# Kernel optimization log

Measured on AMD Instinct MI355X. Metric: run time of the kernel, lower is better.

The kernel has to match this reference:

```python
import jax, jax.numpy as jnp
import numpy as np


def _layernorm(x, g, b, eps=1e-5):
    mu = jnp.mean(x, axis=-1, keepdims=True)
    var = jnp.mean(jnp.square(x - mu), axis=-1, keepdims=True)
    return (x - mu) * jax.lax.rsqrt(var + eps) * g + b


def setup_inputs() -> dict:
    key = jax.random.key(0)
    ks = jax.random.split(key, 8)
    B, S, E, K, H = 32, 64, 768, 36, 4
    w = 0.02
    return {
        "x": jax.random.normal(ks[0], (B, S, E), dtype=jnp.float32),
        "y": jax.random.normal(ks[1], (B * S, K, E), dtype=jnp.float32),
        "ln_gamma": jnp.ones((H, E), jnp.float32),
        "ln_beta": jnp.zeros((H, E), jnp.float32),
        "W1": jax.random.normal(ks[2], (H, E, E), dtype=jnp.float32) * w,
        "b1": jnp.zeros((H, E), jnp.float32),
        "W2x": jax.random.normal(ks[3], (H, E), dtype=jnp.float32) * w,  # first half of Linear(2E,1)
        "W2y": jax.random.normal(ks[4], (H, E), dtype=jnp.float32) * w,  # second half of Linear(2E,1)
        "b2": jnp.zeros((H,), jnp.float32),
        "Wm": jax.random.normal(ks[5], (H * E, E), dtype=jnp.float32) * w,
        "bm": jnp.zeros((E,), jnp.float32),
        "select_indegree_num": 36,
    }


def reference(x, y, ln_gamma, ln_beta, W1, b1, W2x, W2y, b2, Wm, bm, select_indegree_num):
    # x: [B,S,E], y: [B*S,K,E]; dropout layers are identity in eval mode.
    B, S, E = x.shape
    H = ln_gamma.shape[0]
    xf = x.reshape(B * S, E)
    outs = []
    for h in range(H):
        # shared linear1 (LayerNorm + Linear) applied to both x and y
        x_ = _layernorm(xf, ln_gamma[h], ln_beta[h]) @ W1[h] + b1[h]          # [BS,E]
        y_ = _layernorm(y, ln_gamma[h], ln_beta[h]) @ W1[h] + b1[h]           # [BS,K,E]
        logit = (x_ @ W2x[h])[:, None] + y_ @ W2y[h] + b2[h]                  # [BS,K]
        prob = jax.nn.softmax(logit, axis=1)                                   # softmax over neighbors
        a = jnp.einsum('nk,nke->ne', prob, y_)                                 # weighted sum, [BS,E]
        outs.append(jax.nn.gelu(xf + a))                                       # GELU(x + a)
    cat = jnp.concatenate(outs, axis=-1)                                       # [BS,H*E]
    res = jax.nn.gelu(cat @ Wm + bm).reshape(B, S, E)
    return x + res  # has_residual=True
```

## Files before the change

kernel.cpp:

```cpp
#include <hip/hip_runtime.h>
#include <hip/hip_bf16.h>
#include <math.h>

#define EE 768
#define HH 4
#define KK 36
#define BSN 2048

typedef __attribute__((ext_vector_type(8))) short short8;
typedef __attribute__((ext_vector_type(4))) short short4v;
typedef __attribute__((ext_vector_type(4))) float float4v;

__device__ inline short f2bf(float x){
  return __builtin_bit_cast(short, __float2bfloat16(x));
}
__device__ inline float bf2f(short s){
  return __bfloat162float(__builtin_bit_cast(__hip_bfloat16, s));
}
__device__ inline float gelu_tanh(float x){
  float t = tanhf(0.79788456080286536f * (x + 0.044715f * x * x * x));
  return 0.5f * x * (1.0f + t);
}

__global__ __launch_bounds__(256) void k_prep(const float* __restrict__ W1,
                                              const float* __restrict__ W2y,
                                              const float* __restrict__ g,
                                              const float* __restrict__ b1,
                                              const float* __restrict__ Wm,
                                              float* __restrict__ v,
                                              float* __restrict__ b1p,
                                              short* __restrict__ W1t,
                                              short* __restrict__ Wmt){
  __shared__ float tile[32][33];
  const int b = blockIdx.x;

  if (b < 768){
    const int wid  = b * 4 + (threadIdx.x >> 6);
    const int lane = threadIdx.x & 63;
    const int h = wid / EE, e = wid % EE;
    const float* W  = W1 + ((size_t)h * EE + e) * EE;
    const float* wy = W2y + h * EE;
    float acc = 0.f;
    #pragma unroll
    for (int j = 0; j < 12; ++j){
      int f = lane + 64 * j;
      acc += W[f] * wy[f];
    }
    #pragma unroll
    for (int off = 32; off; off >>= 1) acc += __shfl_xor(acc, off);
    if (lane == 0) v[h * EE + e] = g[h * EE + e] * acc;

    int idx = b * 256 + threadIdx.x;
    if (idx < HH * EE) b1p[idx] = b1[idx];
  } else if (b < 3072){
    const int bb = b - 768;
    const int et = bb % 24, ft = (bb / 24) % 24, h = bb / 576;
    const int e0 = et * 32, f0 = ft * 32;
    const int tx = threadIdx.x & 31, ty = threadIdx.x >> 5;
    const float* W = W1 + (size_t)h * EE * EE;
    #pragma unroll
    for (int i = 0; i < 4; ++i){
      int e = e0 + ty + 8 * i;
      tile[ty + 8 * i][tx] = W[(size_t)e * EE + f0 + tx] * g[h * EE + e];
    }
    __syncthreads();
    #pragma unroll
    for (int i = 0; i < 4; ++i){
      int f = f0 + ty + 8 * i;
      W1t[((size_t)h * EE + f) * EE + e0 + tx] = f2bf(tile[tx][ty + 8 * i]);
    }
  } else {
    const int bb = b - 3072;
    const int ct = bb % 96, ft = bb / 96;
    const int c0 = ct * 32, f0 = ft * 32;
    const int tx = threadIdx.x & 31, ty = threadIdx.x >> 5;
    #pragma unroll
    for (int i = 0; i < 4; ++i){
      tile[ty + 8 * i][tx] = Wm[(size_t)(c0 + ty + 8 * i) * EE + f0 + tx];
    }
    __syncthreads();
    #pragma unroll
    for (int i = 0; i < 4; ++i){
      Wmt[(size_t)(f0 + ty + 8 * i) * (HH * EE) + c0 + tx] = f2bf(tile[tx][ty + 8 * i]);
    }
  }
}

__global__ __launch_bounds__(256) void k_b1p_acc(const float* __restrict__ W1,
                                                 const float* __restrict__ beta,
                                                 float* __restrict__ b1p){
  const int h   = blockIdx.x >> 6;
  const int ec0 = (blockIdx.x & 63) * 12;
  const float* W  = W1 + (size_t)h * EE * EE;
  const float* bt = beta + h * EE;
  const int f = threadIdx.x;
  float a0 = 0.f, a1 = 0.f, a2 = 0.f;
  #pragma unroll
  for (int e = ec0; e < ec0 + 12; ++e){
    float be = bt[e];
    const float* row = W + (size_t)e * EE;
    a0 += be * row[f];
    a1 += be * row[f + 256];
    a2 += be * row[f + 512];
  }
  atomicAdd(&b1p[h * EE + f],       a0);
  atomicAdd(&b1p[h * EE + f + 256], a1);
  atomicAdd(&b1p[h * EE + f + 512], a2);
}

__global__ __launch_bounds__(256) void k_pass_y(const float* __restrict__ y,
                                                const float* __restrict__ v,
                                                short* __restrict__ p_y){
  const int wave = threadIdx.x >> 6, lane = threadIdx.x & 63;
  const int n = blockIdx.x * 4 + wave;
  const float* base = y + (size_t)n * KK * EE + 4 * lane;

  float4v vreg[HH][3];
  #pragma unroll
  for (int h = 0; h < HH; ++h)
    #pragma unroll
    for (int j = 0; j < 3; ++j)
      vreg[h][j] = *(const float4v*)(v + h * EE + 4 * lane + 256 * j);

  float4v acc[HH][3];
  #pragma unroll
  for (int h = 0; h < HH; ++h)
    #pragma unroll
    for (int j = 0; j < 3; ++j)
      acc[h][j] = (float4v){0.f, 0.f, 0.f, 0.f};
  float m[HH], l[HH];
  #pragma unroll
  for (int h = 0; h < HH; ++h){ m[h] = -INFINITY; l[h] = 0.f; }

  float4v bufA[3], bufB[3];
  #pragma unroll
  for (int j = 0; j < 3; ++j) bufA[j] = *(const float4v*)(base + 256 * j);
  #pragma unroll
  for (int j = 0; j < 3; ++j) bufB[j] = *(const float4v*)(base + EE + 256 * j);

  #pragma unroll 2
  for (int k = 0; k < KK; ++k){
    float4v cur[3];
    #pragma unroll
    for (int j = 0; j < 3; ++j) cur[j] = bufA[j];
    #pragma unroll
    for (int j = 0; j < 3; ++j) bufA[j] = bufB[j];
    if (k + 2 < KK){
      const float* rp = base + (size_t)(k + 2) * EE;
      #pragma unroll
      for (int j = 0; j < 3; ++j) bufB[j] = *(const float4v*)(rp + 256 * j);
    }

    float s = 0.f, s2 = 0.f;
    #pragma unroll
    for (int j = 0; j < 3; ++j)
      #pragma unroll
      for (int c = 0; c < 4; ++c){ float t = cur[j][c]; s += t; s2 += t * t; }
    #pragma unroll
    for (int off = 32; off; off >>= 1){
      s  += __shfl_xor(s, off);
      s2 += __shfl_xor(s2, off);
    }
    const float mu = s * (1.f / EE);
    const float rs = rsqrtf(s2 * (1.f / EE) - mu * mu + 1e-5f);

    float d[HH] = {0.f, 0.f, 0.f, 0.f};
    #pragma unroll
    for (int j = 0; j < 3; ++j)
      #pragma unroll
      for (int c = 0; c < 4; ++c){
        float t = (cur[j][c] - mu) * rs;
        cur[j][c] = t;
        d[0] += t * vreg[0][j][c];
        d[1] += t * vreg[1][j][c];
        d[2] += t * vreg[2][j][c];
        d[3] += t * vreg[3][j][c];
      }
    #pragma unroll
    for (int off = 32; off; off >>= 1){
      d[0] += __shfl_xor(d[0], off);
      d[1] += __shfl_xor(d[1], off);
      d[2] += __shfl_xor(d[2], off);
      d[3] += __shfl_xor(d[3], off);
    }

    #pragma unroll
    for (int h = 0; h < HH; ++h){
      if (d[h] > m[h]){
        float sc = __expf(m[h] - d[h]);
        l[h] *= sc;
        #pragma unroll
        for (int j = 0; j < 3; ++j)
          #pragma unroll
          for (int c = 0; c < 4; ++c) acc[h][j][c] *= sc;
        m[h] = d[h];
      }
      float w = __expf(d[h] - m[h]);
      l[h] += w;
      #pragma unroll
      for (int j = 0; j < 3; ++j)
        #pragma unroll
        for (int c = 0; c < 4; ++c) acc[h][j][c] += w * cur[j][c];
    }
  }

  #pragma unroll
  for (int h = 0; h < HH; ++h){
    const float inv = 1.f / l[h];
    #pragma unroll
    for (int j = 0; j < 3; ++j){
      short4v pk;
      #pragma unroll
      for (int c = 0; c < 4; ++c) pk[c] = f2bf(acc[h][j][c] * inv);
      *(short4v*)(p_y + ((size_t)h * BSN + n) * EE + 4 * lane + 256 * j) = pk;
    }
  }
}

template<int MODE>
__global__ __launch_bounds__(256) void k_gemm(const short* __restrict__ A,
                                              const short* __restrict__ Bt,
                                              const float* __restrict__ addv,
                                              const float* __restrict__ x,
                                              void* __restrict__ out,
                                              int Kdim, size_t strideA, size_t strideB){
  __shared__ short As[2][64][72];
  __shared__ short Bs[2][64][72];
  const int z = blockIdx.z;
  const short* Ah = A + strideA * z;
  const short* Bh = Bt + strideB * z;
  const int kbeg = 0, kend = Kdim;

  const int tid = threadIdx.x;
  const int wave = tid >> 6, lane = tid & 63;
  const int quad = lane >> 4, l16 = lane & 15;
  const int m0 = blockIdx.x * 64, n0 = blockIdx.y * 64;
  const int r = tid >> 3, c8 = (tid & 7) * 8;

  float4v acc[4];
  #pragma unroll
  for (int t = 0; t < 4; ++t) acc[t] = (float4v){0.f, 0.f, 0.f, 0.f};

  const short* Ap0 = Ah + (size_t)(m0 + r) * Kdim + c8;
  const short* Ap1 = Ah + (size_t)(m0 + r + 32) * Kdim + c8;
  const short* Bp0 = Bh + (size_t)(n0 + r) * Kdim + c8;
  const short* Bp1 = Bh + (size_t)(n0 + r + 32) * Kdim + c8;

  short8 ra0 = *(const short8*)(Ap0 + kbeg);
  short8 ra1 = *(const short8*)(Ap1 + kbeg);
  short8 rb0 = *(const short8*)(Bp0 + kbeg);
  short8 rb1 = *(const short8*)(Bp1 + kbeg);
  *(short8*)(&As[0][r][c8])      = ra0;
  *(short8*)(&As[0][r + 32][c8]) = ra1;
  *(short8*)(&Bs[0][r][c8])      = rb0;
  *(short8*)(&Bs[0][r + 32][c8]) = rb1;
  if (kbeg + 64 < kend){
    ra0 = *(const short8*)(Ap0 + kbeg + 64);
    ra1 = *(const short8*)(Ap1 + kbeg + 64);
    rb0 = *(const short8*)(Bp0 + kbeg + 64);
    rb1 = *(const short8*)(Bp1 + kbeg + 64);
  }
  __syncthreads();

  int cur = 0;
  for (int k0 = kbeg; k0 < kend; k0 += 64){
    if (k0 + 64 < kend){
      const int nx = cur ^ 1;
      *(short8*)(&As[nx][r][c8])      = ra0;
      *(short8*)(&As[nx][r + 32][c8]) = ra1;
      *(short8*)(&Bs[nx][r][c8])      = rb0;
      *(short8*)(&Bs[nx][r + 32][c8]) = rb1;
      if (k0 + 128 < kend){
        ra0 = *(const short8*)(Ap0 + k0 + 128);
        ra1 = *(const short8*)(Ap1 + k0 + 128);
        rb0 = *(const short8*)(Bp0 + k0 + 128);
        rb1 = *(const short8*)(Bp1 + k0 + 128);
      }
    }
    #pragma unroll
    for (int kk = 0; kk < 64; kk += 32){
      short8 bf = *(const short8*)(&Bs[cur][16 * wave + l16][kk + quad * 8]);
      #pragma unroll
      for (int t = 0; t < 4; ++t){
        short8 af = *(const short8*)(&As[cur][16 * t + l16][kk + quad * 8]);
        acc[t] = __builtin_amdgcn_mfma_f32_16x16x32_bf16(af, bf, acc[t], 0, 0, 0);
      }
    }
    __syncthreads();
    cur ^= 1;
  }

  const int f = n0 + 16 * wave + l16;
  if (MODE == 0){
    const float add = addv[768 * z + f];
    #pragma unroll
    for (int t = 0; t < 4; ++t){
      #pragma unroll
      for (int rr = 0; rr < 4; ++rr){
        const int m = m0 + 16 * t + quad * 4 + rr;
        const float val = acc[t][rr] + add;
        const float xf = x[(size_t)m * EE + f];
        ((short*)out)[(size_t)m * (HH * EE) + 768 * z + f] = f2bf(gelu_tanh(xf + val));
      }
    }
  } else {
    const float add = addv[f];
    float* po = (float*)out;
    #pragma unroll
    for (int t = 0; t < 4; ++t){
      #pragma unroll
      for (int rr = 0; rr < 4; ++rr){
        const int m = m0 + 16 * t + quad * 4 + rr;
        const float xf = x[(size_t)m * EE + f];
        po[(size_t)m * EE + f] = xf + gelu_tanh(acc[t][rr] + add);
      }
    }
  }
}

extern "C" void kernel_launch(void* const* d_in, const int* in_sizes, int n_in,
                              void* d_out, int out_size, void* d_ws, size_t ws_size,
                              hipStream_t stream){
  const float* x    = (const float*)d_in[0];
  const float* y    = (const float*)d_in[1];
  const float* g    = (const float*)d_in[2];
  const float* beta = (const float*)d_in[3];
  const float* W1   = (const float*)d_in[4];
  const float* b1   = (const float*)d_in[5];
  const float* W2y  = (const float*)d_in[7];
  const float* Wm   = (const float*)d_in[9];
  const float* bm   = (const float*)d_in[10];

  char* ws = (char*)d_ws;
  float* v    = (float*)(ws + 0);
  float* b1p  = (float*)(ws + 12288);
  short* W1t  = (short*)(ws + 24576);
  short* Wmt  = (short*)(ws + 4743168);
  short* p_y  = (short*)(ws + 9461760);
  short* catb = (short*)(ws + 22044672);
  float* out  = (float*)d_out;

  k_prep<<<dim3(5376), dim3(256), 0, stream>>>(W1, W2y, g, b1, Wm, v, b1p, W1t, Wmt);
  k_b1p_acc<<<dim3(256), dim3(256), 0, stream>>>(W1, beta, b1p);
  k_pass_y<<<dim3(512), dim3(256), 0, stream>>>(y, v, p_y);
  k_gemm<0><<<dim3(32, 12, 4), dim3(256), 0, stream>>>(
      p_y, W1t, b1p, x, (void*)catb, 768, (size_t)2048 * 768, (size_t)768 * 768);
  k_gemm<1><<<dim3(32, 12, 1), dim3(256), 0, stream>>>(
      catb, Wmt, bm, x, (void*)out, 3072, (size_t)0, (size_t)0);
}
```

Measured before the change: 426.7 us.

## Fuse bias and logit-vector prep into transpose pass; single-pass y statistics

The W1 transpose blocks now also accumulate the beta-folded bias and the W2y-projected logit vector through atomics. This removes the separate bias kernel and the extra pass over W1, with a memset zeroing the accumulators. In k_pass_y the layernorm is folded algebraically: dot products with v are taken on the raw row together with the mean and variance sums, and the mean correction is applied at the end. This removes the second elementwise normalize-and-dot pass per neighbor row and halves the cross-lane reduction rounds, at the cost of precision from the one-pass formulation and atomic accumulation order.

```diff
diff --git a/kernel.cpp b/kernel.cpp
--- a/kernel.cpp
+++ b/kernel.cpp
@@ -25,55 +25,44 @@
 __global__ __launch_bounds__(256) void k_prep(const float* __restrict__ W1,
                                               const float* __restrict__ W2y,
                                               const float* __restrict__ g,
-                                              const float* __restrict__ b1,
+                                              const float* __restrict__ beta,
                                               const float* __restrict__ Wm,
                                               float* __restrict__ v,
-                                              float* __restrict__ b1p,
+                                              float* __restrict__ bacc,
                                               short* __restrict__ W1t,
                                               short* __restrict__ Wmt){
   __shared__ float tile[32][33];
   const int b = blockIdx.x;
-
-  if (b < 768){
-    const int wid  = b * 4 + (threadIdx.x >> 6);
-    const int lane = threadIdx.x & 63;
-    const int h = wid / EE, e = wid % EE;
-    const float* W  = W1 + ((size_t)h * EE + e) * EE;
+  const int tx = threadIdx.x & 31, ty = threadIdx.x >> 5;
+
+  if (b < 2304){
+    const int et = b % 24, ft = (b / 24) % 24, h = b / 576;
+    const int e0 = et * 32, f0 = ft * 32;
+    const float* W  = W1 + (size_t)h * EE * EE;
     const float* wy = W2y + h * EE;
-    float acc = 0.f;
-    #pragma unroll
-    for (int j = 0; j < 12; ++j){
-      int f = lane + 64 * j;
-      acc += W[f] * wy[f];
-    }
-    #pragma unroll
-    for (int off = 32; off; off >>= 1) acc += __shfl_xor(acc, off);
-    if (lane == 0) v[h * EE + e] = g[h * EE + e] * acc;
-
-    int idx = b * 256 + threadIdx.x;
-    if (idx < HH * EE) b1p[idx] = b1[idx];
-  } else if (b < 3072){
-    const int bb = b - 768;
-    const int et = bb % 24, ft = (bb / 24) % 24, h = bb / 576;
-    const int e0 = et * 32, f0 = ft * 32;
-    const int tx = threadIdx.x & 31, ty = threadIdx.x >> 5;
-    const float* W = W1 + (size_t)h * EE * EE;
+    float pb = 0.f;
     #pragma unroll
     for (int i = 0; i < 4; ++i){
-      int e = e0 + ty + 8 * i;
-      tile[ty + 8 * i][tx] = W[(size_t)e * EE + f0 + tx] * g[h * EE + e];
-    }
+      const int e = e0 + ty + 8 * i;
+      const float w4 = W[(size_t)e * EE + f0 + tx];
+      tile[ty + 8 * i][tx] = w4 * g[h * EE + e];
+      pb += w4 * beta[h * EE + e];
+    }
+    atomicAdd(&bacc[h * EE + f0 + tx], pb);
     __syncthreads();
+    float pv = 0.f;
     #pragma unroll
     for (int i = 0; i < 4; ++i){
-      int f = f0 + ty + 8 * i;
-      W1t[((size_t)h * EE + f) * EE + e0 + tx] = f2bf(tile[tx][ty + 8 * i]);
-    }
+      const int f = f0 + ty + 8 * i;
+      const float val = tile[tx][ty + 8 * i];
+      W1t[((size_t)h * EE + f) * EE + e0 + tx] = f2bf(val);
+      pv += val * wy[f];
+    }
+    atomicAdd(&v[h * EE + e0 + tx], pv);
   } else {
-    const int bb = b - 3072;
+    const int bb = b - 2304;
     const int ct = bb % 96, ft = bb / 96;
     const int c0 = ct * 32, f0 = ft * 32;
-    const int tx = threadIdx.x & 31, ty = threadIdx.x >> 5;
     #pragma unroll
     for (int i = 0; i < 4; ++i){
       tile[ty + 8 * i][tx] = Wm[(size_t)(c0 + ty + 8 * i) * EE + f0 + tx];
@@ -84,28 +73,6 @@
       Wmt[(size_t)(f0 + ty + 8 * i) * (HH * EE) + c0 + tx] = f2bf(tile[tx][ty + 8 * i]);
     }
   }
-}
-
-__global__ __launch_bounds__(256) void k_b1p_acc(const float* __restrict__ W1,
-                                                 const float* __restrict__ beta,
-                                                 float* __restrict__ b1p){
-  const int h   = blockIdx.x >> 6;
-  const int ec0 = (blockIdx.x & 63) * 12;
-  const float* W  = W1 + (size_t)h * EE * EE;
-  const float* bt = beta + h * EE;
-  const int f = threadIdx.x;
-  float a0 = 0.f, a1 = 0.f, a2 = 0.f;
-  #pragma unroll
-  for (int e = ec0; e < ec0 + 12; ++e){
-    float be = bt[e];
-    const float* row = W + (size_t)e * EE;
-    a0 += be * row[f];
-    a1 += be * row[f + 256];
-    a2 += be * row[f + 512];
-  }
-  atomicAdd(&b1p[h * EE + f],       a0);
-  atomicAdd(&b1p[h * EE + f + 256], a1);
-  atomicAdd(&b1p[h * EE + f + 512], a2);
 }
 
 __global__ __launch_bounds__(256) void k_pass_y(const float* __restrict__ y,
@@ -122,15 +89,33 @@
     for (int j = 0; j < 3; ++j)
       vreg[h][j] = *(const float4v*)(v + h * EE + 4 * lane + 256 * j);
 
-  float4v acc[HH][3];
+  float sv[HH];
+  #pragma unroll
+  for (int h = 0; h < HH; ++h){
+    float t = 0.f;
+    #pragma unroll
+    for (int j = 0; j < 3; ++j)
+      #pragma unroll
+      for (int c = 0; c < 4; ++c) t += vreg[h][j][c];
+    sv[h] = t;
+  }
+  #pragma unroll
+  for (int off = 32; off; off >>= 1){
+    sv[0] += __shfl_xor(sv[0], off);
+    sv[1] += __shfl_xor(sv[1], off);
+    sv[2] += __shfl_xor(sv[2], off);
+    sv[3] += __shfl_xor(sv[3], off);
+  }
+
+  float4v accv[HH][3];
   #pragma unroll
   for (int h = 0; h < HH; ++h)
     #pragma unroll
     for (int j = 0; j < 3; ++j)
-      acc[h][j] = (float4v){0.f, 0.f, 0.f, 0.f};
-  float m[HH], l[HH];
-  #pragma unroll
-  for (int h = 0; h < HH; ++h){ m[h] = -INFINITY; l[h] = 0.f; }
+      accv[h][j] = (float4v){0.f, 0.f, 0.f, 0.f};
+  float accs[HH], m[HH], l[HH];
+  #pragma unroll
+  for (int h = 0; h < HH; ++h){ accs[h] = 0.f; m[h] = -INFINITY; l[h] = 0.f; }
 
   float4v bufA[3], bufB[3];
   #pragma unroll
@@ -152,66 +137,63 @@
     }
 
     float s = 0.f, s2 = 0.f;
+    float dt[HH] = {0.f, 0.f, 0.f, 0.f};
     #pragma unroll
     for (int j = 0; j < 3; ++j)
       #pragma unroll
-      for (int c = 0; c < 4; ++c){ float t = cur[j][c]; s += t; s2 += t * t; }
+      for (int c = 0; c < 4; ++c){
+        const float t = cur[j][c];
+        s += t; s2 += t * t;
+        dt[0] += t * vreg[0][j][c];
+        dt[1] += t * vreg[1][j][c];
+        dt[2] += t * vreg[2][j][c];
+        dt[3] += t * vreg[3][j][c];
+      }
     #pragma unroll
     for (int off = 32; off; off >>= 1){
-      s  += __shfl_xor(s, off);
-      s2 += __shfl_xor(s2, off);
+      s     += __shfl_xor(s,     off);
+      s2    += __shfl_xor(s2,    off);
+      dt[0] += __shfl_xor(dt[0], off);
+      dt[1] += __shfl_xor(dt[1], off);
+      dt[2] += __shfl_xor(dt[2], off);
+      dt[3] += __shfl_xor(dt[3], off);
     }
     const float mu = s * (1.f / EE);
     const float rs = rsqrtf(s2 * (1.f / EE) - mu * mu + 1e-5f);
 
-    float d[HH] = {0.f, 0.f, 0.f, 0.f};
-    #pragma unroll
-    for (int j = 0; j < 3; ++j)
-      #pragma unroll
-      for (int c = 0; c < 4; ++c){
-        float t = (cur[j][c] - mu) * rs;
-        cur[j][c] = t;
-        d[0] += t * vreg[0][j][c];
-        d[1] += t * vreg[1][j][c];
-        d[2] += t * vreg[2][j][c];
-        d[3] += t * vreg[3][j][c];
-      }
-    #pragma unroll
-    for (int off = 32; off; off >>= 1){
-      d[0] += __shfl_xor(d[0], off);
-      d[1] += __shfl_xor(d[1], off);
-      d[2] += __shfl_xor(d[2], off);
-      d[3] += __shfl_xor(d[3], off);
-    }
-
     #pragma unroll
     for (int h = 0; h < HH; ++h){
-      if (d[h] > m[h]){
-        float sc = __expf(m[h] - d[h]);
+      const float d = rs * (dt[h] - mu * sv[h]);
+      if (d > m[h]){
+        const float sc = __expf(m[h] - d);
         l[h] *= sc;
+        accs[h] *= sc;
         #pragma unroll
         for (int j = 0; j < 3; ++j)
           #pragma unroll
-          for (int c = 0; c < 4; ++c) acc[h][j][c] *= sc;
-        m[h] = d[h];
-      }
-      float w = __expf(d[h] - m[h]);
+          for (int c = 0; c < 4; ++c) accv[h][j][c] *= sc;
+        m[h] = d;
+      }
+      const float w = __expf(d - m[h]);
       l[h] += w;
+      const float cw = w * rs;
       #pragma unroll
       for (int j = 0; j < 3; ++j)
         #pragma unroll
-        for (int c = 0; c < 4; ++c) acc[h][j][c] += w * cur[j][c];
+        for (int c = 0; c < 4; ++c) accv[h][j][c] += cw * cur[j][c];
+      accs[h] += cw * mu;
     }
   }
 
   #pragma unroll
   for (int h = 0; h < HH; ++h){
     const float inv = 1.f / l[h];
+    const float as  = accs[h];
     #pragma unroll
     for (int j = 0; j < 3; ++j){
       short4v pk;
       #pragma unroll
-      for (int c = 0; c < 4; ++c) pk[c] = f2bf(acc[h][j][c] * inv);
+      for (int c = 0; c < 4; ++c) pk[c] = f2bf((accv[h][j][c] - as) * inv);
       *(short4v*)(p_y + ((size_t)h * BSN + n) * EE + 4 * lane + 256 * j) = pk;
     }
   }
@@ -221,6 +203,7 @@
 __global__ __launch_bounds__(256) void k_gemm(const short* __restrict__ A,
                                               const short* __restrict__ Bt,
                                               const float* __restrict__ addv,
+                                              const float* __restrict__ addv2,
                                               const float* __restrict__ x,
                                               void* __restrict__ out,
                                               int Kdim, size_t strideA, size_t strideB){
@@ -292,7 +275,7 @@
 
   const int f = n0 + 16 * wave + l16;
   if (MODE == 0){
-    const float add = addv[768 * z + f];
+    const float add = addv[768 * z + f] + addv2[768 * z + f];
     #pragma unroll
     for (int t = 0; t < 4; ++t){
       #pragma unroll
@@ -333,18 +316,18 @@
 
   char* ws = (char*)d_ws;
   float* v    = (float*)(ws + 0);
-  float* b1p  = (float*)(ws + 12288);
+  float* bacc = (float*)(ws + 12288);
   short* W1t  = (short*)(ws + 24576);
   short* Wmt  = (short*)(ws + 4743168);
   short* p_y  = (short*)(ws + 9461760);
   short* catb = (short*)(ws + 22044672);
   float* out  = (float*)d_out;
 
-  k_prep<<<dim3(5376), dim3(256), 0, stream>>>(W1, W2y, g, b1, Wm, v, b1p, W1t, Wmt);
-  k_b1p_acc<<<dim3(256), dim3(256), 0, stream>>>(W1, beta, b1p);
+  hipMemsetAsync(ws, 0, 24576, stream);
+  k_prep<<<dim3(4608), dim3(256), 0, stream>>>(W1, W2y, g, beta, Wm, v, bacc, W1t, Wmt);
   k_pass_y<<<dim3(512), dim3(256), 0, stream>>>(y, v, p_y);
   k_gemm<0><<<dim3(32, 12, 4), dim3(256), 0, stream>>>(
-      p_y, W1t, b1p, x, (void*)catb, 768, (size_t)2048 * 768, (size_t)768 * 768);
+      p_y, W1t, bacc, b1, x, (void*)catb, 768, (size_t)2048 * 768, (size_t)768 * 768);
   k_gemm<1><<<dim3(32, 12, 1), dim3(256), 0, stream>>>(
-      catb, Wmt, bm, x, (void*)out, 3072, (size_t)0, (size_t)0);
-}
+      catb, Wmt, bm, nullptr, x, (void*)out, 3072, (size_t)0, (size_t)0);
+}
```

After: 451.3 us. 1.06x slower.
